# Kernel optimization log

Measured on AMD Instinct MI355X. Metric: run time of the kernel, lower is better.

Reference implementation:

```python
import jax, jax.numpy as jnp
import numpy as np
from jax import lax

B, CIN, L, COUT, K = 64, 64, 4096, 128, 7
STRIDE, PAD = 1, 3
POOL, POOL_STRIDE = 2, 2
BN_EPS = 1e-5


def setup_inputs() -> dict:
    key = jax.random.key(0)
    ks = jax.random.split(key, 7)
    I = jax.random.normal(ks[0], (B, CIN, L), jnp.float32)
    bn_gamma = 1.0 + 0.1 * jax.random.normal(ks[1], (CIN,), jnp.float32)
    bn_beta = 0.1 * jax.random.normal(ks[2], (CIN,), jnp.float32)
    bn_mean = 0.1 * jax.random.normal(ks[3], (CIN,), jnp.float32)
    bn_var = jax.random.uniform(ks[4], (CIN,), jnp.float32, 0.5, 1.5)
    conv_w = 0.05 * jax.random.normal(ks[5], (COUT, CIN, K), jnp.float32)
    # XNOR-Net style per-output-channel scale alpha = mean(|W|) over (Cin, K)
    alpha = jnp.mean(jnp.abs(conv_w), axis=(1, 2))  # [COUT]
    prelu_w = jnp.full((1,), 0.25, jnp.float32)  # nn.PReLU() default: 1 shared param
    return dict(I=I, bn_gamma=bn_gamma, bn_beta=bn_beta, bn_mean=bn_mean,
                bn_var=bn_var, conv_w=conv_w, alpha=alpha, prelu_w=prelu_w)


def reference(I, bn_gamma, bn_beta, bn_mean, bn_var, conv_w, alpha, prelu_w):
    # BatchNorm1d (eval mode: running stats), per-channel over dim 1
    scale = (bn_gamma / jnp.sqrt(bn_var + BN_EPS))[None, :, None]
    x = (I - bn_mean[None, :, None]) * scale + bn_beta[None, :, None]
    # Binarize (sign; sign(0)=0 matches torch.sign)
    x = jnp.sign(x)
    # Conv1d, no bias, zero padding=3, stride=1  -> [B, COUT, L]
    y = lax.conv_general_dilated(x, conv_w, window_strides=(STRIDE,),
                                 padding=[(PAD, PAD)],
                                 dimension_numbers=('NCH', 'OIH', 'NCH'))
    # alpha scale (per output channel)
    y = y * alpha[None, :, None]
    # PReLU with single shared parameter
    y = jnp.where(y > 0, y, prelu_w[0] * y)
    # MaxPool1d(kernel=2, stride=2)
    y = lax.reduce_window(y, -jnp.inf, lax.max,
                          (1, 1, POOL), (1, 1, POOL_STRIDE), 'VALID')
    return y
```

## Files before the change

### kernel.cpp

```cpp
#include <hip/hip_runtime.h>
#include <hip/hip_bf16.h>
#include <stdint.h>

#define BATCH 64
#define CIN   64
#define LEN   4096
#define COUT  128
#define KW    7
#define LPOOL 2048
#define NT    4
#define RROWS 72
#define RAWP  80
#define SPITCH 64

typedef __bf16 v8bf __attribute__((ext_vector_type(8)));
typedef unsigned short v8us __attribute__((ext_vector_type(8)));
typedef float  v4f  __attribute__((ext_vector_type(4)));

typedef const __attribute__((address_space(1))) void* gp1_t;
typedef __attribute__((address_space(3))) void* lp3_t;

__global__ __launch_bounds__(256)
void wconv_kernel(const float* __restrict__ W, ushort* __restrict__ Wt) {
    int i = blockIdx.x * 256 + threadIdx.x;
    if (i >= COUT * CIN * KW) return;
    int co  = i / (CIN * KW);
    int rem = i - co * (CIN * KW);
    int ci  = rem / KW;
    int k   = rem - ci * KW;
    uint u = __float_as_uint(W[i]);
    uint r = (u + 0x7FFFu + ((u >> 16) & 1u)) >> 16;
    Wt[(k * COUT + co) * CIN + ci] = (ushort)r;
}

__global__ __launch_bounds__(256, 3)
void conv_kernel(const float* __restrict__ I,
                 const float* __restrict__ bn_g, const float* __restrict__ bn_b,
                 const float* __restrict__ bn_m, const float* __restrict__ bn_v,
                 const ushort* __restrict__ Wt,
                 const float* __restrict__ alpha, const float* __restrict__ prelu,
                 float* __restrict__ out) {
    __shared__ __attribute__((aligned(16))) float  raw[CIN * RAWP];
    __shared__ __attribute__((aligned(16))) ushort stg[RROWS * SPITCH];

    int tid = threadIdx.x;
    int lane = tid & 63, wave = tid >> 6;
    int b = blockIdx.y, bx = blockIdx.x;
    int l0base = bx * (64 * NT);

    const float* Ib = I + (size_t)b * CIN * LEN;

    const char* gb[5]; int cb[5];
    #pragma unroll
    for (int i = 0; i < 5; ++i) {
        int n = (wave * 5 + i) * 64 + lane;
        int ci = n / 20;
        int c  = n - 20 * ci;
        cb[i] = 16 * c - 32;
        gb[i] = (const char*)(Ib + (size_t)ci * LEN) + cb[i];
    }

    {
        int l4 = 4 * l0base;
        #pragma unroll
        for (int i = 0; i < 5; ++i) {
            int off = cb[i] + l4;
            if (off >= 0 && off + 16 <= LEN * 4)
                __builtin_amdgcn_global_load_lds((gp1_t)(gb[i] + l4),
                                                 (lp3_t)(raw + (wave * 5 + i) * 256), 16, 0, 0);
        }
    }

    int brq  = tid >> 3;
    int bg8  = tid & 7;
    int bci0 = bg8 * 8;
    float sc[8], mn[8], bt[8];
    if (tid < 144) {
        #pragma unroll
        for (int c = 0; c < 8; ++c) {
            int ci = bci0 + c;
            sc[c] = __fdiv_rn(bn_g[ci], __fsqrt_rn(__fadd_rn(bn_v[ci], 1e-5f)));
            mn[c] = bn_m[ci];
            bt[c] = bn_b[ci];
        }
    }

    int quad = lane >> 4, lr = lane & 15;
    int cout0 = wave * 32;
    const ushort* wbase = Wt + ((size_t)cout0 + lr) * CIN + quad * 8;
    float pw  = prelu[0];
    float al0 = alpha[cout0 + lr];
    float al1 = alpha[cout0 + 16 + lr];
    float* obase = out + ((size_t)b * COUT) * LPOOL + bx * (32 * NT);

    v8bf c00 = *(const v8bf*)(wbase);
    v8bf c01 = *(const v8bf*)(wbase + 16 * CIN);
    v8bf c10 = *(const v8bf*)(wbase + 32);
    v8bf c11 = *(const v8bf*)(wbase + 32 + 16 * CIN);

    __syncthreads();

    const float4* raw4 = (const float4*)raw;

    for (int t = 0; t < NT; ++t) {
        int l0 = l0base + t * 64;

        if (tid < 144) {
            float4 fr[8];
            #pragma unroll
            for (int c = 0; c < 8; ++c)
                fr[c] = raw4[(bci0 + c) * (RAWP / 4) + brq + 1];
            #pragma unroll
            for (int j = 0; j < 4; ++j) {
                int r = 4 * brq + j;
                int p = l0 - 4 + r;
                bool pok = (p >= 0) && (p < LEN);
                v8us u;
                #pragma unroll
                for (int c = 0; c < 8; ++c) {
                    float v = ((const float*)&fr[c])[j];
                    float x = __fadd_rn(__fmul_rn(__fsub_rn(v, mn[c]), sc[c]), bt[c]);
                    ushort s = x > 0.f ? (ushort)0x3F80 : (x < 0.f ? (ushort)0xBF80 : (ushort)0);
                    u[c] = pok ? s : (ushort)0;
                }
                *(v8us*)(&stg[r * SPITCH + ((bg8 ^ (r & 7)) << 3)]) = u;
            }
        }
        __syncthreads();

        if (t + 1 < NT) {
            int l4 = 4 * (l0 + 64);
            #pragma unroll
            for (int i = 0; i < 5; ++i) {
                int off = cb[i] + l4;
                if (off >= 0 && off + 16 <= LEN * 4)
                    __builtin_amdgcn_global_load_lds((gp1_t)(gb[i] + l4),
                                                     (lp3_t)(raw + (wave * 5 + i) * 256), 16, 0, 0);
            }
        }

        v4f acc[4][2];
        #pragma unroll
        for (int mt = 0; mt < 4; ++mt) { acc[mt][0] = (v4f)0.f; acc[mt][1] = (v4f)0.f; }

        #pragma unroll 1
        for (int k = 0; k < KW; ++k) {
            int nk = (k == KW - 1) ? 0 : k + 1;
            const ushort* wn = wbase + nk * COUT * CIN;
            v8bf n00 = *(const v8bf*)(wn);
            v8bf n01 = *(const v8bf*)(wn + 16 * CIN);
            v8bf n10 = *(const v8bf*)(wn + 32);
            v8bf n11 = *(const v8bf*)(wn + 32 + 16 * CIN);

            int rk = lr + 1 + k;
            int s8 = rk & 7;
            const ushort* a0p = &stg[rk * SPITCH + ((quad ^ s8) << 3)];
            const ushort* a1p = &stg[rk * SPITCH + (((quad ^ 4) ^ s8) << 3)];
            #pragma unroll
            for (int mt = 0; mt < 4; ++mt) {
                v8bf a0 = *(const v8bf*)(a0p + mt * 16 * SPITCH);
                v8bf a1 = *(const v8bf*)(a1p + mt * 16 * SPITCH);
                acc[mt][0] = __builtin_amdgcn_mfma_f32_16x16x32_bf16(a0, c00, acc[mt][0], 0, 0, 0);
                acc[mt][1] = __builtin_amdgcn_mfma_f32_16x16x32_bf16(a0, c01, acc[mt][1], 0, 0, 0);
                acc[mt][0] = __builtin_amdgcn_mfma_f32_16x16x32_bf16(a1, c10, acc[mt][0], 0, 0, 0);
                acc[mt][1] = __builtin_amdgcn_mfma_f32_16x16x32_bf16(a1, c11, acc[mt][1], 0, 0, 0);
            }
            c00 = n00; c01 = n01; c10 = n10; c11 = n11;
        }

        float* ob = obase + t * 32;
        #pragma unroll
        for (int n2 = 0; n2 < 2; ++n2) {
            float al = n2 ? al1 : al0;
            int co = cout0 + n2 * 16 + lr;
            float* oc = ob + (size_t)co * LPOOL + quad * 2;
            #pragma unroll
            for (int mt = 0; mt < 4; ++mt) {
                float v0 = acc[mt][n2][0] * al; v0 = v0 > 0.f ? v0 : pw * v0;
                float v1 = acc[mt][n2][1] * al; v1 = v1 > 0.f ? v1 : pw * v1;
                float v2 = acc[mt][n2][2] * al; v2 = v2 > 0.f ? v2 : pw * v2;
                float v3 = acc[mt][n2][3] * al; v3 = v3 > 0.f ? v3 : pw * v3;
                *(float2*)(oc + mt * 8) = make_float2(fmaxf(v0, v1), fmaxf(v2, v3));
            }
        }
        __syncthreads();
    }
}

extern "C" void kernel_launch(void* const* d_in, const int* in_sizes, int n_in,
                              void* d_out, int out_size, void* d_ws, size_t ws_size,
                              hipStream_t stream) {
    const float* I      = (const float*)d_in[0];
    const float* bn_g   = (const float*)d_in[1];
    const float* bn_b   = (const float*)d_in[2];
    const float* bn_m   = (const float*)d_in[3];
    const float* bn_v   = (const float*)d_in[4];
    const float* conv_w = (const float*)d_in[5];
    const float* alpha  = (const float*)d_in[6];
    const float* prelu  = (const float*)d_in[7];
    float* out = (float*)d_out;

    ushort* Wt = (ushort*)d_ws;

    wconv_kernel<<<(COUT * CIN * KW + 255) / 256, 256, 0, stream>>>(conv_w, Wt);
    dim3 grid(LEN / (64 * NT), BATCH);
    conv_kernel<<<grid, 256, 0, stream>>>(I, bn_g, bn_b, bn_m, bn_v, Wt, alpha, prelu, out);
}
```

Baseline: 177.8 us.

## Double-buffer binarized tile and give each wave its own input slice

Each wave now DMAs and binarizes its own 16-channel slice of the input, so the asynchronous load can be waited on per wave with vmcnt instead of a block barrier. The staged bf16 tile is double-buffered, and the next tile is binarized after the MFMA loop and before the output stores, leaving one barrier per iteration instead of two. This removes a block-wide sync and lets binarization overlap with other waves' compute. In exchange it doubles the staging LDS, relies on hand-placed waitcnt asm for correctness, and spreads binarization over more waves, each with fewer active lanes.

```diff
diff --git a/kernel.cpp b/kernel.cpp
--- a/kernel.cpp
+++ b/kernel.cpp
@@ -33,6 +33,14 @@
     Wt[(k * COUT + co) * CIN + ci] = (ushort)r;
 }
 
+static __device__ __forceinline__ void sync_lds() {
+    asm volatile("s_waitcnt lgkmcnt(0)" ::: "memory");
+    __builtin_amdgcn_s_barrier();
+}
+static __device__ __forceinline__ void wait_vm0() {
+    asm volatile("s_waitcnt vmcnt(0)" ::: "memory");
+}
+
 __global__ __launch_bounds__(256, 3)
 void conv_kernel(const float* __restrict__ I,
                  const float* __restrict__ bn_g, const float* __restrict__ bn_b,
@@ -41,7 +49,7 @@
                  const float* __restrict__ alpha, const float* __restrict__ prelu,
                  float* __restrict__ out) {
     __shared__ __attribute__((aligned(16))) float  raw[CIN * RAWP];
-    __shared__ __attribute__((aligned(16))) ushort stg[RROWS * SPITCH];
+    __shared__ __attribute__((aligned(16))) ushort stg[2][RROWS * SPITCH];
 
     int tid = threadIdx.x;
     int lane = tid & 63, wave = tid >> 6;
@@ -50,35 +58,38 @@
 
     const float* Ib = I + (size_t)b * CIN * LEN;
 
+    float* rawb = raw + wave * 1280;
     const char* gb[5]; int cb[5];
     #pragma unroll
     for (int i = 0; i < 5; ++i) {
-        int n = (wave * 5 + i) * 64 + lane;
-        int ci = n / 20;
-        int c  = n - 20 * ci;
+        int m = i * 64 + lane;
+        int cil = m / 20;
+        int c   = m - 20 * cil;
         cb[i] = 16 * c - 32;
-        gb[i] = (const char*)(Ib + (size_t)ci * LEN) + cb[i];
+        gb[i] = (const char*)(Ib + (size_t)(16 * wave + cil) * LEN) + cb[i];
     }
 
-    {
-        int l4 = 4 * l0base;
+    auto dma_tile = [&](int l0t) {
+        int l4 = 4 * l0t;
         #pragma unroll
         for (int i = 0; i < 5; ++i) {
             int off = cb[i] + l4;
             if (off >= 0 && off + 16 <= LEN * 4)
                 __builtin_amdgcn_global_load_lds((gp1_t)(gb[i] + l4),
-                                                 (lp3_t)(raw + (wave * 5 + i) * 256), 16, 0, 0);
-        }
-    }
-
-    int brq  = tid >> 3;
-    int bg8  = tid & 7;
-    int bci0 = bg8 * 8;
+                                                 (lp3_t)(rawb + i * 256), 16, 0, 0);
+        }
+    };
+
+    dma_tile(l0base);
+
+    int oc  = lane & 1;
+    int brq = lane >> 1;
+    int g8  = 2 * wave + oc;
     float sc[8], mn[8], bt[8];
-    if (tid < 144) {
+    if (lane < 36) {
         #pragma unroll
         for (int c = 0; c < 8; ++c) {
-            int ci = bci0 + c;
+            int ci = 8 * g8 + c;
             sc[c] = __fdiv_rn(bn_g[ci], __fsqrt_rn(__fadd_rn(bn_v[ci], 1e-5f)));
             mn[c] = bn_m[ci];
             bt[c] = bn_b[ci];
@@ -98,22 +109,18 @@
     v8bf c10 = *(const v8bf*)(wbase + 32);
     v8bf c11 = *(const v8bf*)(wbase + 32 + 16 * CIN);
 
-    __syncthreads();
-
-    const float4* raw4 = (const float4*)raw;
-
-    for (int t = 0; t < NT; ++t) {
-        int l0 = l0base + t * 64;
-
-        if (tid < 144) {
+    auto binarize = [&](int l0t, int buf) {
+        if (lane < 36) {
+            const float4* r4 = (const float4*)rawb;
             float4 fr[8];
             #pragma unroll
             for (int c = 0; c < 8; ++c)
-                fr[c] = raw4[(bci0 + c) * (RAWP / 4) + brq + 1];
+                fr[c] = r4[(8 * oc + c) * 20 + brq + 1];
+            ushort* sb = &stg[buf][0];
             #pragma unroll
             for (int j = 0; j < 4; ++j) {
                 int r = 4 * brq + j;
-                int p = l0 - 4 + r;
+                int p = l0t - 4 + r;
                 bool pok = (p >= 0) && (p < LEN);
                 v8us u;
                 #pragma unroll
@@ -123,21 +130,19 @@
                     ushort s = x > 0.f ? (ushort)0x3F80 : (x < 0.f ? (ushort)0xBF80 : (ushort)0);
                     u[c] = pok ? s : (ushort)0;
                 }
-                *(v8us*)(&stg[r * SPITCH + ((bg8 ^ (r & 7)) << 3)]) = u;
+                *(v8us*)(&sb[r * SPITCH + ((g8 ^ (r & 7)) << 3)]) = u;
             }
         }
-        __syncthreads();
-
-        if (t + 1 < NT) {
-            int l4 = 4 * (l0 + 64);
-            #pragma unroll
-            for (int i = 0; i < 5; ++i) {
-                int off = cb[i] + l4;
-                if (off >= 0 && off + 16 <= LEN * 4)
-                    __builtin_amdgcn_global_load_lds((gp1_t)(gb[i] + l4),
-                                                     (lp3_t)(raw + (wave * 5 + i) * 256), 16, 0, 0);
-            }
-        }
+    };
+
+    wait_vm0();
+    binarize(l0base, 0);
+    if (NT > 1) dma_tile(l0base + 64);
+    sync_lds();
+
+    for (int t = 0; t < NT; ++t) {
+        int l0 = l0base + t * 64;
+        const ushort* sb_cur = &stg[t & 1][0];
 
         v4f acc[4][2];
         #pragma unroll
@@ -154,8 +159,8 @@
 
             int rk = lr + 1 + k;
             int s8 = rk & 7;
-            const ushort* a0p = &stg[rk * SPITCH + ((quad ^ s8) << 3)];
-            const ushort* a1p = &stg[rk * SPITCH + (((quad ^ 4) ^ s8) << 3)];
+            const ushort* a0p = &sb_cur[rk * SPITCH + ((quad ^ s8) << 3)];
+            const ushort* a1p = &sb_cur[rk * SPITCH + (((quad ^ 4) ^ s8) << 3)];
             #pragma unroll
             for (int mt = 0; mt < 4; ++mt) {
                 v8bf a0 = *(const v8bf*)(a0p + mt * 16 * SPITCH);
@@ -168,22 +173,38 @@
             c00 = n00; c01 = n01; c10 = n10; c11 = n11;
         }
 
-        float* ob = obase + t * 32;
+        float pv[2][4][2];
         #pragma unroll
         for (int n2 = 0; n2 < 2; ++n2) {
             float al = n2 ? al1 : al0;
-            int co = cout0 + n2 * 16 + lr;
-            float* oc = ob + (size_t)co * LPOOL + quad * 2;
             #pragma unroll
             for (int mt = 0; mt < 4; ++mt) {
                 float v0 = acc[mt][n2][0] * al; v0 = v0 > 0.f ? v0 : pw * v0;
                 float v1 = acc[mt][n2][1] * al; v1 = v1 > 0.f ? v1 : pw * v1;
                 float v2 = acc[mt][n2][2] * al; v2 = v2 > 0.f ? v2 : pw * v2;
                 float v3 = acc[mt][n2][3] * al; v3 = v3 > 0.f ? v3 : pw * v3;
-                *(float2*)(oc + mt * 8) = make_float2(fmaxf(v0, v1), fmaxf(v2, v3));
+                pv[n2][mt][0] = fmaxf(v0, v1);
+                pv[n2][mt][1] = fmaxf(v2, v3);
             }
         }
-        __syncthreads();
+
+        if (t + 1 < NT) {
+            wait_vm0();
+            binarize(l0 + 64, (t + 1) & 1);
+        }
+        if (t + 2 < NT) dma_tile(l0 + 128);
+
+        float* ob = obase + t * 32;
+        #pragma unroll
+        for (int n2 = 0; n2 < 2; ++n2) {
+            int co = cout0 + n2 * 16 + lr;
+            float* ocp = ob + (size_t)co * LPOOL + quad * 2;
+            #pragma unroll
+            for (int mt = 0; mt < 4; ++mt)
+                *(float2*)(ocp + mt * 8) = make_float2(pv[n2][mt][0], pv[n2][mt][1]);
+        }
+
+        sync_lds();
     }
 }
 
```

Measured after the change: 191.4 us. 7.6% more time.
